# Kernel optimization log

Measured on AMD Instinct MI355X. Metric: run time of the kernel, lower is better.

## Reference

```python
import jax, jax.numpy as jnp
import numpy as np

STRIDES = (8.0, 16.0, 32.0)


def _decode_level(feat, W, b, stride, level):
    # feat: [bs, C, ny, nx]; W: [85, C]; b: [85]
    bs, _, ny, nx = feat.shape
    # 1x1 conv == channel contraction; output laid out as [bs, ny, nx, 85]
    p = jnp.einsum('bchw,oc->bhwo', feat, W) + b
    y = jax.nn.sigmoid(p)
    xv = jnp.arange(nx, dtype=y.dtype)            # broadcasts over last spatial dim
    yv = jnp.arange(ny, dtype=y.dtype)[:, None]   # broadcasts over row dim
    power = jnp.asarray(2.0 ** level, dtype=y.dtype)
    d = (y[..., :4] * 2.0) ** 2 * power           # dx1, dy1, dx2, dy2
    x1 = (xv + 1.0 - d[..., 0]) * stride
    y1 = (yv + 1.0 - d[..., 1]) * stride
    x2 = (xv + d[..., 2]) * stride
    y2 = (yv + d[..., 3]) * stride
    # xyxy -> xywh
    box = jnp.stack([(x1 + x2) * 0.5, (y1 + y2) * 0.5, x2 - x1, y2 - y1], axis=-1)
    out = jnp.concatenate([box, y[..., 4:]], axis=-1)  # [bs, ny, nx, 85]
    return out.reshape(bs, ny * nx, out.shape[-1])


def setup_inputs() -> dict:
    key = jax.random.key(0)
    ks = jax.random.split(key, 9)
    f32 = jnp.float32
    return {
        'x0': jax.random.normal(ks[0], (16, 256, 80, 80), dtype=f32),
        'x1': jax.random.normal(ks[1], (16, 512, 40, 40), dtype=f32),
        'x2': jax.random.normal(ks[2], (16, 1024, 20, 20), dtype=f32),
        'W0': jax.random.normal(ks[3], (85, 256), dtype=f32) * 0.05,
        'b0': jax.random.normal(ks[4], (85,), dtype=f32) * 0.05,
        'W1': jax.random.normal(ks[5], (85, 512), dtype=f32) * 0.05,
        'b1': jax.random.normal(ks[6], (85,), dtype=f32) * 0.05,
        'W2': jax.random.normal(ks[7], (85, 1024), dtype=f32) * 0.05,
        'b2': jax.random.normal(ks[8], (85,), dtype=f32) * 0.05,
    }


def reference(x0, x1, x2, W0, b0, W1, b1, W2, b2):
    feats = (x0, x1, x2)
    Ws = (W0, W1, W2)
    bs_ = (b0, b1, b2)
    z = [_decode_level(feats[i], Ws[i], bs_[i], STRIDES[i], i) for i in range(3)]
    return jnp.concatenate(z, axis=1)  # [bs, 8400, 85]
```

## Files before the change

kernel.cpp:

```cpp
#include <hip/hip_runtime.h>
#include <cstdint>


typedef __attribute__((ext_vector_type(8))) short bf16x8;
typedef __attribute__((ext_vector_type(4))) float f32x4;

constexpr int KS0 = 8, KS1 = 16, KS2 = 32;
constexpr int F0 = 6 * KS0, F1 = 6 * KS1, F2 = 6 * KS2;
constexpr int FOFF0 = 0, FOFF1 = F0, FOFF2 = F0 + F1;
constexpr int NFRAG = F0 + F1 + F2;
constexpr size_t BIAS_OFF = 0;
constexpr size_t BPK_OFF  = 1152;
constexpr size_t WS_NEED  = BPK_OFF + (size_t)NFRAG * 64 * 16;

__device__ __forceinline__ unsigned short f2bf(float f) {
    union { float f; unsigned u; } v; v.f = f;
    unsigned r = v.u + 0x7FFF + ((v.u >> 16) & 1);
    return (unsigned short)(r >> 16);
}

__device__ __forceinline__ void barrier_keep_vmcnt() {
    asm volatile("s_waitcnt lgkmcnt(0)" ::: "memory");
    __builtin_amdgcn_s_barrier();
}

__global__ __launch_bounds__(256) void prep_pack(
    const float* __restrict__ W0, const float* __restrict__ W1,
    const float* __restrict__ W2,
    const float* __restrict__ b0, const float* __restrict__ b1,
    const float* __restrict__ b2,
    unsigned char* __restrict__ ws)
{
    int t = blockIdx.x * 256 + threadIdx.x;
    if (t < 288) {
        int lvl = t / 96, o = t % 96;
        const float* bp = (lvl == 0) ? b0 : (lvl == 1) ? b1 : b2;
        ((float*)(ws + BIAS_OFF))[t] = (o < 85) ? bp[o] : 0.0f;
    }
    if (t >= NFRAG * 64) return;
    int frag = t >> 6, l = t & 63;
    int C; const float* W; int f;
    if (frag < FOFF1)      { C = 256;  W = W0; f = frag;         }
    else if (frag < FOFF2) { C = 512;  W = W1; f = frag - FOFF1; }
    else                   { C = 1024; W = W2; f = frag - FOFF2; }
    int ks = f / 6, n = f % 6;
    int o  = n * 16 + (l & 15);
    int c0 = ks * 32 + (l >> 4) * 8;
    bf16x8 r;
#pragma unroll
    for (int e = 0; e < 8; ++e)
        r[e] = (o < 85) ? (short)f2bf(W[(size_t)o * C + c0 + e]) : (short)0;
    ((bf16x8*)(ws + BPK_OFF))[frag * 64 + l] = r;
}

template <int C, int HW, int NX, int LEVEL, int AOFF, int KSTEPS, int FOFF>
__device__ __forceinline__ void mfma_level(
    const float* __restrict__ feat, const unsigned char* __restrict__ ws,
    float* __restrict__ out, int blk, uint4* __restrict__ Bsm )
{
    const int tid = threadIdx.x;
    const int w   = tid >> 6;
    const int l   = tid & 63;
    const int col = l & 15;
    const int kg  = l >> 4;
    const bool lo_half = (tid < 128);

    const int p0  = blk * 64 + w * 16;
    const int b   = p0 / HW;
    const int hw0 = p0 - b * HW;
    const float* fb = feat + (size_t)b * C * HW + hw0;
    const float* pA = fb + col + (size_t)(kg * 8) * HW;

    const float* bias = (const float*)(ws + BIAS_OFF) + LEVEL * 96;
    const uint4* bsrc = (const uint4*)(ws + BPK_OFF) + (size_t)FOFF * 64;

    f32x4 acc[6];
#pragma unroll
    for (int n = 0; n < 6; ++n) {
        float bv = bias[n * 16 + col];
        f32x4 z = { bv, bv, bv, bv };
        acc[n] = z;
    }

    uint4* buf0 = Bsm;
    uint4* buf1 = Bsm + 384;

    {
        const uint4* s = bsrc;
        buf0[tid] = s[tid];
        if (lo_half) buf0[256 + tid] = s[256 + tid];
    }
    float flA0[8], flA1[8];
#pragma unroll
    for (int e = 0; e < 8; ++e) flA0[e] = pA[(size_t)e * HW];
    if (KSTEPS > 1) {
        const float* p = pA + (size_t)32 * HW;
#pragma unroll
        for (int e = 0; e < 8; ++e) flA1[e] = p[(size_t)e * HW];
    }
    uint4 pb0, pb1;
    if (KSTEPS > 1) {
        const uint4* s = bsrc + 384;
        pb0 = s[tid];
        if (lo_half) pb1 = s[256 + tid];
    }
    barrier_keep_vmcnt();

#pragma unroll 1
    for (int ks = 0; ks < KSTEPS; ks += 2) {
        if (ks + 1 < KSTEPS) {
            buf1[tid] = pb0;
            if (lo_half) buf1[256 + tid] = pb1;
        }
        if (ks + 2 < KSTEPS) {
            const uint4* s = bsrc + (size_t)(ks + 2) * 384;
            pb0 = s[tid];
            if (lo_half) pb1 = s[256 + tid];
        }
        {
            bf16x8 a;
#pragma unroll
            for (int e = 0; e < 8; ++e) a[e] = (short)f2bf(flA0[e]);
            if (ks + 2 < KSTEPS) {
                const float* p = pA + (size_t)((ks + 2) * 32) * HW;
#pragma unroll
                for (int e = 0; e < 8; ++e) flA0[e] = p[(size_t)e * HW];
            }
            const bf16x8* bl = (const bf16x8*)buf0;
#pragma unroll
            for (int n = 0; n < 6; ++n) {
                bf16x8 bq = bl[n * 64 + l];
                acc[n] = __builtin_amdgcn_mfma_f32_16x16x32_bf16(a, bq, acc[n], 0, 0, 0);
            }
        }
        barrier_keep_vmcnt();

        if (ks + 2 < KSTEPS) {
            buf0[tid] = pb0;
            if (lo_half) buf0[256 + tid] = pb1;
        }
        if (ks + 3 < KSTEPS) {
            const uint4* s = bsrc + (size_t)(ks + 3) * 384;
            pb0 = s[tid];
            if (lo_half) pb1 = s[256 + tid];
        }
        if (ks + 1 < KSTEPS) {
            bf16x8 a;
#pragma unroll
            for (int e = 0; e < 8; ++e) a[e] = (short)f2bf(flA1[e]);
            if (ks + 3 < KSTEPS) {
                const float* p = pA + (size_t)((ks + 3) * 32) * HW;
#pragma unroll
                for (int e = 0; e < 8; ++e) flA1[e] = p[(size_t)e * HW];
            }
            const bf16x8* bl = (const bf16x8*)buf1;
#pragma unroll
            for (int n = 0; n < 6; ++n) {
                bf16x8 bq = bl[n * 64 + l];
                acc[n] = __builtin_amdgcn_mfma_f32_16x16x32_bf16(a, bq, acc[n], 0, 0, 0);
            }
        }
        barrier_keep_vmcnt();
    }

    constexpr float S  = (float)(8 << LEVEL);
    constexpr float P4 = 4.0f * (float)(1 << LEVEL);
#pragma unroll
    for (int j = 0; j < 4; ++j) {
        const int hw = hw0 + kg * 4 + j;
        float sg[6];
#pragma unroll
        for (int n = 0; n < 6; ++n) {
            float v = acc[n][j];
            sg[n] = __builtin_amdgcn_rcpf(1.0f + __expf(-v));
        }
        const int grp = l & 48;
        float y0 = __shfl(sg[0], grp + 0);
        float y1 = __shfl(sg[0], grp + 1);
        float y2 = __shfl(sg[0], grp + 2);
        float y3 = __shfl(sg[0], grp + 3);
        float wx = (float)(hw % NX);
        float wy = (float)(hw / NX);
        float d0 = y0 * y0 * P4, d1 = y1 * y1 * P4;
        float d2 = y2 * y2 * P4, d3 = y3 * y3 * P4;
        float x1 = (wx + 1.0f - d0) * S;
        float yA = (wy + 1.0f - d1) * S;
        float x2 = (wx + d2) * S;
        float yB = (wy + d3) * S;
        float bx = (x1 + x2) * 0.5f, by = (yA + yB) * 0.5f;
        float bw = x2 - x1,          bh = yB - yA;
        sg[0] = (col == 0) ? bx : (col == 1) ? by
              : (col == 2) ? bw : (col == 3) ? bh : sg[0];
        float* op = out + ((size_t)b * 8400 + AOFF + hw) * 85;
#pragma unroll
        for (int n = 0; n < 6; ++n) {
            int o = n * 16 + col;
            if (o < 85) op[o] = sg[n];
        }
    }
}

__global__ __launch_bounds__(256, 6) void detect_mfma(
    const float* __restrict__ x0, const float* __restrict__ x1,
    const float* __restrict__ x2,
    const unsigned char* __restrict__ ws, float* __restrict__ out)
{
    __shared__ uint4 Bsm[2 * 384];
    int blk = blockIdx.x;
    if (blk < 100)      mfma_level<1024, 400,  20, 2, 8000, KS2, FOFF2>(x2, ws, out, blk,       Bsm);
    else if (blk < 500) mfma_level<512,  1600, 40, 1, 6400, KS1, FOFF1>(x1, ws, out, blk - 100, Bsm);
    else                mfma_level<256,  6400, 80, 0, 0,    KS0, FOFF0>(x0, ws, out, blk - 500, Bsm);
}

template <int C, int HW, int NX, int LEVEL, int ONUM, bool BOX>
__device__ __forceinline__ void decode_path_fb(
    const float* __restrict__ feat, const float* __restrict__ Wm,
    const float* __restrict__ bias, float* __restrict__ out,
    int o_lo_in, int pos)
{
    const int o_lo = __builtin_amdgcn_readfirstlane(o_lo_in);
    const int b  = pos / HW;
    const int hw = pos - b * HW;
    const float* fp = feat + (size_t)b * (C * HW) + hw;
    float acc[ONUM];
#pragma unroll
    for (int j = 0; j < ONUM; ++j) acc[j] = bias[o_lo + j];
#pragma unroll 4
    for (int c = 0; c < C; ++c) {
        float fv = fp[(size_t)c * HW];
#pragma unroll
        for (int j = 0; j < ONUM; ++j)
            acc[j] = fmaf(fv, Wm[(o_lo + j) * C + c], acc[j]);
    }
#pragma unroll
    for (int j = 0; j < ONUM; ++j)
        acc[j] = __builtin_amdgcn_rcpf(1.0f + __expf(-acc[j]));
    constexpr float S = (float)(8 << LEVEL);
    constexpr int AOFF = (LEVEL == 0) ? 0 : ((LEVEL == 1) ? 6400 : 8000);
    float* op = out + ((size_t)b * 8400 + AOFF + hw) * 85 + o_lo;
    if constexpr (BOX) {
        constexpr float P4 = 4.0f * (float)(1 << LEVEL);
        float wx = (float)(hw % NX), wy = (float)(hw / NX);
        float d0 = acc[0] * acc[0] * P4, d1 = acc[1] * acc[1] * P4;
        float d2 = acc[2] * acc[2] * P4, d3 = acc[3] * acc[3] * P4;
        float x1 = (wx + 1.0f - d0) * S, y1 = (wy + 1.0f - d1) * S;
        float x2 = (wx + d2) * S,        y2 = (wy + d3) * S;
        op[0] = (x1 + x2) * 0.5f; op[1] = (y1 + y2) * 0.5f;
        op[2] = x2 - x1;          op[3] = y2 - y1;
#pragma unroll
        for (int j = 4; j < ONUM; ++j) op[j] = acc[j];
    } else {
#pragma unroll
        for (int j = 0; j < ONUM; ++j) op[j] = acc[j];
    }
}

template <int C, int HW, int NX, int LEVEL>
__device__ __forceinline__ void level_block_fb(
    const float* __restrict__ feat, const float* __restrict__ Wm,
    const float* __restrict__ bias, float* __restrict__ out, int bb)
{
    const int wave = threadIdx.x >> 6, lane = threadIdx.x & 63;
    const int pos = bb * 64 + lane;
    if      (wave == 0) decode_path_fb<C, HW, NX, LEVEL, 22, true >(feat, Wm, bias, out, 0,  pos);
    else if (wave == 1) decode_path_fb<C, HW, NX, LEVEL, 22, false>(feat, Wm, bias, out, 22, pos);
    else if (wave == 2) decode_path_fb<C, HW, NX, LEVEL, 22, false>(feat, Wm, bias, out, 44, pos);
    else                decode_path_fb<C, HW, NX, LEVEL, 19, false>(feat, Wm, bias, out, 66, pos);
}

__global__ __launch_bounds__(256) void detect_fallback(
    const float* __restrict__ x0, const float* __restrict__ x1,
    const float* __restrict__ x2,
    const float* __restrict__ w0, const float* __restrict__ w1,
    const float* __restrict__ w2,
    const float* __restrict__ b0, const float* __restrict__ b1,
    const float* __restrict__ b2, float* __restrict__ out)
{
    const int blk = blockIdx.x;
    if (blk < 100)      level_block_fb<1024, 400,  20, 2>(x2, w2, b2, out, blk);
    else if (blk < 500) level_block_fb<512,  1600, 40, 1>(x1, w1, b1, out, blk - 100);
    else                level_block_fb<256,  6400, 80, 0>(x0, w0, b0, out, blk - 500);
}

extern "C" void kernel_launch(void* const* d_in, const int* in_sizes, int n_in,
                              void* d_out, int out_size, void* d_ws, size_t ws_size,
                              hipStream_t stream)
{
    const float* x0 = (const float*)d_in[0];
    const float* x1 = (const float*)d_in[1];
    const float* x2 = (const float*)d_in[2];
    const float* W0 = (const float*)d_in[3];
    const float* b0 = (const float*)d_in[4];
    const float* W1 = (const float*)d_in[5];
    const float* b1 = (const float*)d_in[6];
    const float* W2 = (const float*)d_in[7];
    const float* b2 = (const float*)d_in[8];
    float* out = (float*)d_out;

    if (ws_size >= WS_NEED) {
        unsigned char* ws = (unsigned char*)d_ws;
        prep_pack<<<(NFRAG * 64 + 255) / 256, 256, 0, stream>>>(W0, W1, W2, b0, b1, b2, ws);
        detect_mfma<<<2100, 256, 0, stream>>>(x0, x1, x2, ws, out);
    } else {
        detect_fallback<<<2100, 256, 0, stream>>>(x0, x1, x2, W0, W1, W2, b0, b1, b2, out);
    }
}
```

Baseline: 48.34 us.

## Process two K-steps per barrier with double-buffered paired B tiles in LDS

Restructures the MFMA main loop so each iteration stages two K-steps of packed weights (768 uint4) into LDS and runs 12 MFMAs between barriers, halving the number of workgroup barriers. The loop now swaps two buffers of paired stages instead of alternating single-stage buffers. LDS use doubles to 24 KB per block, which can reduce occupancy, and more registers are held for prefetched weights.

```diff
diff --git a/kernel.cpp b/kernel.cpp
--- a/kernel.cpp
+++ b/kernel.cpp
@@ -58,12 +58,12 @@
     const float* __restrict__ feat, const unsigned char* __restrict__ ws,
     float* __restrict__ out, int blk, uint4* __restrict__ Bsm )
 {
+    constexpr int NP = KSTEPS / 2;
     const int tid = threadIdx.x;
     const int w   = tid >> 6;
     const int l   = tid & 63;
     const int col = l & 15;
     const int kg  = l >> 4;
-    const bool lo_half = (tid < 128);
 
     const int p0  = blk * 64 + w * 16;
     const int b   = p0 / HW;
@@ -82,85 +82,76 @@
         acc[n] = z;
     }
 
-    uint4* buf0 = Bsm;
-    uint4* buf1 = Bsm + 384;
+    uint4* bufc = Bsm;
+    uint4* bufn = Bsm + 768;
 
     {
         const uint4* s = bsrc;
-        buf0[tid] = s[tid];
-        if (lo_half) buf0[256 + tid] = s[256 + tid];
+        bufc[tid]       = s[tid];
+        bufc[256 + tid] = s[256 + tid];
+        bufc[512 + tid] = s[512 + tid];
     }
     float flA0[8], flA1[8];
 #pragma unroll
     for (int e = 0; e < 8; ++e) flA0[e] = pA[(size_t)e * HW];
-    if (KSTEPS > 1) {
+    {
         const float* p = pA + (size_t)32 * HW;
 #pragma unroll
         for (int e = 0; e < 8; ++e) flA1[e] = p[(size_t)e * HW];
     }
-    uint4 pb0, pb1;
-    if (KSTEPS > 1) {
-        const uint4* s = bsrc + 384;
+    uint4 pb0, pb1, pb2;
+    if (NP > 1) {
+        const uint4* s = bsrc + 768;
         pb0 = s[tid];
-        if (lo_half) pb1 = s[256 + tid];
+        pb1 = s[256 + tid];
+        pb2 = s[512 + tid];
     }
     barrier_keep_vmcnt();
 
 #pragma unroll 1
-    for (int ks = 0; ks < KSTEPS; ks += 2) {
-        if (ks + 1 < KSTEPS) {
-            buf1[tid] = pb0;
-            if (lo_half) buf1[256 + tid] = pb1;
-        }
-        if (ks + 2 < KSTEPS) {
-            const uint4* s = bsrc + (size_t)(ks + 2) * 384;
+    for (int p = 0; p < NP; ++p) {
+        bf16x8 a0, a1;
+#pragma unroll
+        for (int e = 0; e < 8; ++e) a0[e] = (short)f2bf(flA0[e]);
+#pragma unroll
+        for (int e = 0; e < 8; ++e) a1[e] = (short)f2bf(flA1[e]);
+
+        if (p + 1 < NP) {
+            const float* q0 = pA + (size_t)((2 * p + 2) * 32) * HW;
+            const float* q1 = pA + (size_t)((2 * p + 3) * 32) * HW;
+#pragma unroll
+            for (int e = 0; e < 8; ++e) flA0[e] = q0[(size_t)e * HW];
+#pragma unroll
+            for (int e = 0; e < 8; ++e) flA1[e] = q1[(size_t)e * HW];
+        }
+
+        if (p + 1 < NP) {
+            bufn[tid]       = pb0;
+            bufn[256 + tid] = pb1;
+            bufn[512 + tid] = pb2;
+        }
+        if (p + 2 < NP) {
+            const uint4* s = bsrc + (size_t)(p + 2) * 768;
             pb0 = s[tid];
-            if (lo_half) pb1 = s[256 + tid];
-        }
-        {
-            bf16x8 a;
-#pragma unroll
-            for (int e = 0; e < 8; ++e) a[e] = (short)f2bf(flA0[e]);
-            if (ks + 2 < KSTEPS) {
-                const float* p = pA + (size_t)((ks + 2) * 32) * HW;
-#pragma unroll
-                for (int e = 0; e < 8; ++e) flA0[e] = p[(size_t)e * HW];
-            }
-            const bf16x8* bl = (const bf16x8*)buf0;
-#pragma unroll
-            for (int n = 0; n < 6; ++n) {
-                bf16x8 bq = bl[n * 64 + l];
-                acc[n] = __builtin_amdgcn_mfma_f32_16x16x32_bf16(a, bq, acc[n], 0, 0, 0);
-            }
-        }
+            pb1 = s[256 + tid];
+            pb2 = s[512 + tid];
+        }
+
+        const bf16x8* bl0 = (const bf16x8*)bufc;
+        const bf16x8* bl1 = (const bf16x8*)(bufc + 384);
+#pragma unroll
+        for (int n = 0; n < 6; ++n) {
+            bf16x8 bq = bl0[n * 64 + l];
+            acc[n] = __builtin_amdgcn_mfma_f32_16x16x32_bf16(a0, bq, acc[n], 0, 0, 0);
+        }
+#pragma unroll
+        for (int n = 0; n < 6; ++n) {
+            bf16x8 bq = bl1[n * 64 + l];
+            acc[n] = __builtin_amdgcn_mfma_f32_16x16x32_bf16(a1, bq, acc[n], 0, 0, 0);
+        }
+
         barrier_keep_vmcnt();
-
-        if (ks + 2 < KSTEPS) {
-            buf0[tid] = pb0;
-            if (lo_half) buf0[256 + tid] = pb1;
-        }
-        if (ks + 3 < KSTEPS) {
-            const uint4* s = bsrc + (size_t)(ks + 3) * 384;
-            pb0 = s[tid];
-            if (lo_half) pb1 = s[256 + tid];
-        }
-        if (ks + 1 < KSTEPS) {
-            bf16x8 a;
-#pragma unroll
-            for (int e = 0; e < 8; ++e) a[e] = (short)f2bf(flA1[e]);
-            if (ks + 3 < KSTEPS) {
-                const float* p = pA + (size_t)((ks + 3) * 32) * HW;
-#pragma unroll
-                for (int e = 0; e < 8; ++e) flA1[e] = p[(size_t)e * HW];
-            }
-            const bf16x8* bl = (const bf16x8*)buf1;
-#pragma unroll
-            for (int n = 0; n < 6; ++n) {
-                bf16x8 bq = bl[n * 64 + l];
-                acc[n] = __builtin_amdgcn_mfma_f32_16x16x32_bf16(a, bq, acc[n], 0, 0, 0);
-            }
-        }
-        barrier_keep_vmcnt();
+        uint4* t = bufc; bufc = bufn; bufn = t;
     }
 
     constexpr float S  = (float)(8 << LEVEL);
@@ -205,7 +196,7 @@
     const float* __restrict__ x2,
     const unsigned char* __restrict__ ws, float* __restrict__ out)
 {
-    __shared__ uint4 Bsm[2 * 384];
+    __shared__ uint4 Bsm[2 * 768];
     int blk = blockIdx.x;
     if (blk < 100)      mfma_level<1024, 400,  20, 2, 8000, KS2, FOFF2>(x2, ws, out, blk,       Bsm);
     else if (blk < 500) mfma_level<512,  1600, 40, 1, 6400, KS1, FOFF1>(x1, ws, out, blk - 100, Bsm);
```

After: 59.21 us. +22.5%, slower.
